# Kernel optimization log

Hardware: AMD Instinct MI355X
Metric: run time of the kernel (lower is better)

## Reference

```python
import jax, jax.numpy as jnp
import numpy as np
import math

EPS = 1e-6
TEMPERATURE = 1.0
NEG = -100.0


def setup_inputs() -> dict:
    key = jax.random.key(0)
    k1, k2, k3 = jax.random.split(key, 3)
    B, N, C = 16, 2048, 64
    x = jax.random.normal(k1, (B, N, C), dtype=jnp.float32)
    y = jax.random.normal(k2, (B, N, C), dtype=jnp.float32)
    # complementary keep / pruned gates, as produced by the TPS token scorer
    keep = jax.random.bernoulli(k3, 0.5, (B, N, 1)).astype(jnp.float32)
    pruned = 1.0 - keep
    return {
        "x": x,
        "y": y,
        "current_keep_decision": keep,
        "current_pruned_decision": pruned,
    }


def reference(x, y, current_keep_decision, current_pruned_decision):
    # Training branch of TPSModule.forward (module defaults to training mode).
    B, N, C = x.shape
    # --- get_sim(x, None, mask_eye=-100, l2_norm=True) ---
    xn = x / (jnp.linalg.norm(x, axis=-1, keepdims=True) + EPS)
    sim = jnp.einsum("bnc,bmc->bnm", xn, xn)  # [B, N, N]
    eye = jnp.eye(N, dtype=bool)
    sim = jnp.where(eye[None, :, :], NEG, sim)
    sim = sim / TEMPERATURE
    # mask out columns of non-kept tokens
    keep_b = current_keep_decision.reshape(B, 1, N).astype(bool)
    sim = jnp.where(keep_b, sim, NEG)
    # hard top-1 (with ties) per row, gated by pruned flag of the source row
    sim_th = jnp.max(sim, axis=2, keepdims=True)  # [B, N, 1]
    mask = (sim == sim_th).astype(x.dtype) * current_pruned_decision  # [B, N, N]
    cos = mask * sim
    # transpose: now rows index destination (kept) tokens
    mask_t = mask.transpose(0, 2, 1)
    cos_t = cos.transpose(0, 2, 1)
    numerator = jnp.exp(cos_t) * mask_t  # [B, N, N]
    denominator = math.e + jnp.sum(numerator, axis=-1, keepdims=True)  # [B, N, 1]
    out = x * (math.e / denominator) + jnp.einsum(
        "bnm,bmc->bnc", numerator / denominator, x
    )
    return out
```

## Files before the change

### kernel.cpp

```cpp
#include <hip/hip_runtime.h>
#include <math.h>

#define BB 16
#define NN 2048
#define CC 64
#define TPB 256
#define MROWS 16
#define RPW 4
#define E_CONST 2.71828182845904523536f

__global__ __launch_bounds__(TPB) void k_pre(const float* __restrict__ keep,
                                             float* __restrict__ outz,
                                             float* __restrict__ S,
                                             int* __restrict__ cntP,
                                             int* __restrict__ cntK,
                                             int* __restrict__ listP,
                                             int* __restrict__ listK) {
    const int tid = threadIdx.x, lane = tid & 63;

    float4* o4 = (float4*)outz + (size_t)blockIdx.x * 1024;
    float4 z = {0.0f, 0.0f, 0.0f, 0.0f};
#pragma unroll
    for (int i = 0; i < 4; ++i) o4[i * TPB + tid] = z;

    const int b = blockIdx.x;
    if (b >= BB) return;

    __shared__ int cP, cK;
    if (tid == 0) { cP = 0; cK = 0; }
    __syncthreads();
    for (int i = tid; i < NN; i += TPB) S[b * NN + i] = 0.0f;
    const unsigned long long lt = (lane == 63) ? 0x7fffffffffffffffull
                                               : ((1ull << lane) - 1ull);
#pragma unroll
    for (int it = 0; it < NN / TPB; ++it) {
        int n = it * TPB + tid;
        bool kp = keep[b * NN + n] != 0.0f;
        unsigned long long mk = __ballot(kp);
        int nk = __popcll(mk);
        int bk = 0, bp = 0;
        if (lane == 0) {
            bk = atomicAdd(&cK, nk);
            bp = atomicAdd(&cP, 64 - nk);
        }
        bk = __shfl(bk, 0); bp = __shfl(bp, 0);
        int pk = __popcll(mk & lt);
        if (kp) listK[b * NN + bk + pk] = n;
        else    listP[b * NN + bp + (lane - pk)] = n;
    }
    __syncthreads();
    if (tid == 0) { cntP[b] = cP; cntK[b] = cK; }
}

__global__ __launch_bounds__(TPB) void k_pre2(const float* __restrict__ x,
                                              const int* __restrict__ cntK,
                                              const int* __restrict__ listK,
                                              float* __restrict__ colMf) {
    const int b    = blockIdx.x & 15;
    const int seg  = blockIdx.x >> 4;
    const int lane = threadIdx.x & 63;
    const int wid  = threadIdx.x >> 6;
    const int wave = seg * 4 + wid;
    const int K    = cntK[b];
    const int Kend = min(NN, K + 128);

    const float* xb = x + (size_t)b * NN * CC;
    float* cf = colMf + (size_t)b * 16 * NN * 4;

    for (int colp = wave; colp < Kend; colp += 256) {
        float v = 0.0f;
        if (colp < K) {
            int tok = listK[b * NN + colp];
            float xv = xb[(size_t)tok * CC + lane];
            float sq = xv * xv;
#pragma unroll
            for (int off = 32; off; off >>= 1) sq += __shfl_xor(sq, off, 64);
            v = xv / (sqrtf(sq) + 1e-6f);
        }
        cf[((size_t)(lane >> 2) * NN + colp) * 4 + (lane & 3)] = v;
    }
}

template <int J>
__device__ __forceinline__ void tile_body(const float4* __restrict__ x4,
                                          const float4* __restrict__ cm,
                                          const int* rtok, int cstart, int K,
                                          int lane, float* tmax,
                                          unsigned long long* msk) {
    float acc[RPW][J];
#pragma unroll
    for (int r = 0; r < RPW; ++r)
#pragma unroll
        for (int j = 0; j < J; ++j) acc[r][j] = 0.0f;

#pragma unroll 2
    for (int k4 = 0; k4 < 16; ++k4) {
        float4 rv[RPW];
#pragma unroll
        for (int r = 0; r < RPW; ++r)
            rv[r] = x4[(size_t)rtok[r] * 16 + k4];
        const float4* cmk = cm + (size_t)k4 * NN + cstart + lane;
        float4 cv[J];
#pragma unroll
        for (int j = 0; j < J; ++j)
            cv[j] = cmk[j * 64];
#pragma unroll
        for (int r = 0; r < RPW; ++r)
#pragma unroll
            for (int j = 0; j < J; ++j)
                acc[r][j] = fmaf(rv[r].x, cv[j].x,
                            fmaf(rv[r].y, cv[j].y,
                            fmaf(rv[r].z, cv[j].z,
                            fmaf(rv[r].w, cv[j].w, acc[r][j]))));
    }

    const int cb0 = cstart >> 6;
#pragma unroll
    for (int r = 0; r < RPW; ++r)
#pragma unroll
        for (int j = 0; j < J; ++j) {
            int colp = cstart + j * 64 + lane;
            float s = (colp < K) ? acc[r][j] : -1.0e30f;
            unsigned long long bit = 1ull << (cb0 + j);
            if (s > tmax[r])       { tmax[r] = s; msk[r] = bit; }
            else if (s == tmax[r])  msk[r] |= bit;
        }
}

__global__ __launch_bounds__(TPB, 4) void k_argmax(
    const float* __restrict__ x,
    const float4* __restrict__ colM,
    const int*   __restrict__ cntP,
    const int*   __restrict__ cntK,
    const int*   __restrict__ listP,
    const int*   __restrict__ listK,
    float* __restrict__ S,
    float* __restrict__ A) {

    const int b    = blockIdx.x & 15;
    const int tile = blockIdx.x >> 4;
    const int P = cntP[b], K = cntK[b];
    const int base = tile * MROWS;
    if (base >= P) return;

    const int tid = threadIdx.x;
    const int wid = tid >> 6;
    const int lane = tid & 63;

    int rtok[RPW];
#pragma unroll
    for (int r = 0; r < RPW; ++r) {
        int rid = base + wid * RPW + r;
        int tok = (rid < P) ? listP[b * NN + rid] : 0;
        rtok[r] = __builtin_amdgcn_readfirstlane(tok);
    }
    const float4* x4 = (const float4*)(x + (size_t)b * NN * CC);
    const float4* cm = colM + (size_t)b * 16 * NN;

    float              tmax[RPW];
    unsigned long long msk[RPW];
#pragma unroll
    for (int r = 0; r < RPW; ++r) { tmax[r] = -3.0e38f; msk[r] = 0ull; }

    int cstart = 0;
    while (cstart < K) {
        int rem = K - cstart;
        if (rem > 384) {
            tile_body<8>(x4, cm, rtok, cstart, K, lane, tmax, msk);
            cstart += 512;
        } else if (rem > 128) {
            tile_body<4>(x4, cm, rtok, cstart, K, lane, tmax, msk);
            cstart += 256;
        } else {
            tile_body<2>(x4, cm, rtok, cstart, K, lane, tmax, msk);
            cstart += 128;
        }
    }

    int nvr = P - base - wid * RPW;
    for (int r = 0; r < RPW; ++r) {
        if (r >= nvr) break;
        float m = tmax[r];
#pragma unroll
        for (int off = 32; off; off >>= 1) m = fmaxf(m, __shfl_xor(m, off, 64));
        int src = rtok[r];
        float xv = x[(size_t)(b * NN + src) * CC + lane];
        float sq = xv * xv;
#pragma unroll
        for (int off = 32; off; off >>= 1) sq += __shfl_xor(sq, off, 64);
        float ivr = 1.0f / (sqrtf(sq) + 1e-6f);
        float wgt = expf(m * ivr);
        unsigned long long bal = __ballot(tmax[r] == m && msk[r] != 0ull);
        while (bal) {
            int sl = __ffsll(bal) - 1;
            bal &= bal - 1;
            unsigned long long mm = __shfl(msk[r], sl);
            while (mm) {
                int cb = __ffsll(mm) - 1;
                mm &= mm - 1;
                int colp = (cb << 6) + sl;
                int dst = listK[b * NN + colp];
                atomicAdd(&A[(size_t)(b * NN + dst) * CC + lane], wgt * xv);
                if (lane == 0) atomicAdd(&S[b * NN + dst], wgt);
            }
        }
    }
}

__global__ __launch_bounds__(TPB) void k_finalize(const float* __restrict__ x,
                                                  const float* __restrict__ S,
                                                  float* __restrict__ out) {
    int i = blockIdx.x * TPB + threadIdx.x;
    int row = i >> 4;
    float inv = 1.0f / (E_CONST + S[row]);
    float4 xv = ((const float4*)x)[i];
    float4 av = ((float4*)out)[i];
    float4 o;
    o.x = (xv.x * E_CONST + av.x) * inv;
    o.y = (xv.y * E_CONST + av.y) * inv;
    o.z = (xv.z * E_CONST + av.z) * inv;
    o.w = (xv.w * E_CONST + av.w) * inv;
    ((float4*)out)[i] = o;
}

extern "C" void kernel_launch(void* const* d_in, const int* in_sizes, int n_in,
                              void* d_out, int out_size, void* d_ws, size_t ws_size,
                              hipStream_t stream) {
    const float* x    = (const float*)d_in[0];
    const float* keep = (const float*)d_in[2];
    float* out = (float*)d_out;

    char* ws = (char*)d_ws;
    float* S    = (float*)(ws + (128 << 10));
    int*   cntP = (int*)(ws + (256 << 10));
    int*   cntK = cntP + 16;
    int*   listP = (int*)(ws + (256 << 10) + 128);
    int*   listK = listP + BB * NN;
    float* colMf = (float*)(ws + (1 << 20));

    k_pre<<<512, TPB, 0, stream>>>(keep, out, S, cntP, cntK, listP, listK);

    k_pre2<<<BB * 64, TPB, 0, stream>>>(x, cntK, listK, colMf);

    k_argmax<<<(NN / MROWS) * BB, TPB, 0, stream>>>(x, (const float4*)colMf,
                                                    cntP, cntK, listP, listK,
                                                    S, out);

    k_finalize<<<(BB * NN * CC / 4) / TPB, TPB, 0, stream>>>(x, S, out);
}
```

Baseline: 140.6 us.

## Halve rows per wave in argmax and stage column-matrix writes through LDS

The argmax kernel now processes 2 rows per wave (8 per block) instead of 4, and its launch bound asks for 8 blocks per CU. This lowers register pressure, raises occupancy and doubles the number of blocks so the work spreads more evenly, at the cost of reloading column tiles twice as often per row. The normalization prep kernel now has each block handle 64 columns: it writes normalized vectors into shared memory and then emits coalesced float4 stores in the transposed layout, replacing the scattered strided global writes. The prep launch shrinks to 512 blocks, and blocks beyond the needed column range return early.

```diff
diff --git a/kernel.cpp b/kernel.cpp
--- a/kernel.cpp
+++ b/kernel.cpp
@@ -5,8 +5,8 @@
 #define NN 2048
 #define CC 64
 #define TPB 256
-#define MROWS 16
-#define RPW 4
+#define MROWS 8
+#define RPW 2
 #define E_CONST 2.71828182845904523536f
 
 __global__ __launch_bounds__(TPB) void k_pre(const float* __restrict__ keep,
@@ -56,18 +56,22 @@
                                               const int* __restrict__ cntK,
                                               const int* __restrict__ listK,
                                               float* __restrict__ colMf) {
-    const int b    = blockIdx.x & 15;
-    const int seg  = blockIdx.x >> 4;
+    const int b     = blockIdx.x & 15;
+    const int chunk = blockIdx.x >> 4;
+    const int base  = chunk * 64;
+    const int K     = cntK[b];
+    const int Kend  = min(NN, K + 128);
+    if (base >= Kend) return;
+
+    __shared__ float lds[64][68];
     const int lane = threadIdx.x & 63;
     const int wid  = threadIdx.x >> 6;
-    const int wave = seg * 4 + wid;
-    const int K    = cntK[b];
-    const int Kend = min(NN, K + 128);
-
     const float* xb = x + (size_t)b * NN * CC;
-    float* cf = colMf + (size_t)b * 16 * NN * 4;
-
-    for (int colp = wave; colp < Kend; colp += 256) {
+
+#pragma unroll
+    for (int i = 0; i < 16; ++i) {
+        int cl = wid * 16 + i;
+        int colp = base + cl;
         float v = 0.0f;
         if (colp < K) {
             int tok = listK[b * NN + colp];
@@ -77,7 +81,22 @@
             for (int off = 32; off; off >>= 1) sq += __shfl_xor(sq, off, 64);
             v = xv / (sqrtf(sq) + 1e-6f);
         }
-        cf[((size_t)(lane >> 2) * NN + colp) * 4 + (lane & 3)] = v;
+        lds[cl][lane] = v;
+    }
+    __syncthreads();
+
+    float4* cm4 = (float4*)colMf + (size_t)b * 16 * NN;
+    const int c  = threadIdx.x & 63;
+    const int kg = threadIdx.x >> 6;
+#pragma unroll
+    for (int g = 0; g < 4; ++g) {
+        int k4 = kg * 4 + g;
+        float4 f;
+        f.x = lds[c][k4 * 4 + 0];
+        f.y = lds[c][k4 * 4 + 1];
+        f.z = lds[c][k4 * 4 + 2];
+        f.w = lds[c][k4 * 4 + 3];
+        cm4[(size_t)k4 * NN + base + c] = f;
     }
 }
 
@@ -127,7 +146,7 @@
         }
 }
 
-__global__ __launch_bounds__(TPB, 4) void k_argmax(
+__global__ __launch_bounds__(TPB, 8) void k_argmax(
     const float* __restrict__ x,
     const float4* __restrict__ colM,
     const int*   __restrict__ cntP,
@@ -240,7 +259,7 @@
 
     k_pre<<<512, TPB, 0, stream>>>(keep, out, S, cntP, cntK, listP, listK);
 
-    k_pre2<<<BB * 64, TPB, 0, stream>>>(x, cntK, listK, colMf);
+    k_pre2<<<512, TPB, 0, stream>>>(x, cntK, listK, colMf);
 
     k_argmax<<<(NN / MROWS) * BB, TPB, 0, stream>>>(x, (const float4*)colMf,
                                                     cntP, cntK, listP, listK,
```

Result: slower. 178.1 us (+26.6%).
